# Performance work log

Hardware: AMD Instinct MI355X
Metric: run time of the kernel (lower is better)

The kernel has to match this reference:

```python
import jax, jax.numpy as jnp
import numpy as np

N_NODES = 50000
N_EDGES = 500000
IN_DIM = 64
OUT_DIM = 64
NUM_RELS = 16


def setup_inputs() -> dict:
    key = jax.random.key(0)
    ks = jax.random.split(key, 8)
    h = jax.random.normal(ks[0], (N_NODES, IN_DIM), dtype=jnp.float32)
    he = jax.random.normal(ks[1], (N_EDGES, IN_DIM), dtype=jnp.float32)
    src = jax.random.randint(ks[2], (N_EDGES,), 0, N_NODES)
    dst = jax.random.randint(ks[3], (N_EDGES,), 0, N_NODES)
    rel = jax.random.randint(ks[4], (N_EDGES,), 0, NUM_RELS)
    # xavier-ish scales
    W_shared = jax.random.normal(ks[5], (OUT_DIM, IN_DIM), dtype=jnp.float32) * (2.0 / (IN_DIM + OUT_DIM)) ** 0.5
    W_attn = jax.random.normal(ks[6], (1, 3 * OUT_DIM), dtype=jnp.float32) * (2.0 / (3 * OUT_DIM + 1)) ** 0.5
    W_rel = jax.random.normal(ks[7], (NUM_RELS, IN_DIM, OUT_DIM), dtype=jnp.float32) * (2.0 / (IN_DIM + OUT_DIM)) ** 0.5
    return {"h": h, "he": he, "src": src, "dst": dst, "rel": rel,
            "W_shared": W_shared, "W_attn": W_attn, "W_rel": W_rel}


def reference(h, he, src, dst, rel, W_shared, W_attn, W_rel):
    # --- edge attention: a = attn_fc([z_src, z_edge, z_dst]) (raw linear score, no softmax in original) ---
    Z = h @ W_shared.T                      # [N, out] project all nodes once
    ze = he @ W_shared.T                    # [E, out]
    # split attn weight to avoid materializing [E, 3*out] concat
    Wa_s, Wa_e, Wa_d = jnp.split(W_attn, 3, axis=1)   # each [1, out]
    a = Z[src] @ Wa_s.T + ze @ Wa_e.T + Z[dst] @ Wa_d.T   # [E, 1]
    # --- message: msg = (h_src @ W_rel[rel]) * a ---
    # compute per-(node, relation) transform once [N, R, out], then gather per edge
    H_all = jnp.einsum('ni,rio->nro', h, W_rel)          # [N, R, out]
    msg = H_all[src, rel] * a                             # [E, out]
    # --- scatter-sum aggregation into destination nodes ---
    out = jax.ops.segment_sum(msg, dst, num_segments=N_NODES)  # [N, out]
    # apply_func: activation (relu), no bias
    return jax.nn.relu(out)
```

## Files before the change

### kernel.cpp

```cpp
#include <hip/hip_runtime.h>
#include <math.h>

#define N_NODES 50000
#define N_EDGES 500000
#define DIM 64
#define NUM_RELS 16
#define GPB 160


__global__ void k1_node(const float* __restrict__ h,
                        const float* __restrict__ W_shared,
                        const float* __restrict__ W_attn,
                        float* __restrict__ sn, float* __restrict__ dn,
                        float4* __restrict__ out4,
                        int* __restrict__ counts, int* __restrict__ cursor) {
    __shared__ float sus[64], sud[64];
    int t = threadIdx.x;
    if (t < 64) {
        float us = 0.f, ud = 0.f;
        for (int o = 0; o < 64; ++o) {
            float w = W_shared[o * 64 + t];
            us = fmaf(w, W_attn[o],       us);
            ud = fmaf(w, W_attn[128 + o], ud);
        }
        sus[t] = us; sud[t] = ud;
    }
    if (t >= 64 && t < 80)  counts[t - 64] = 0;
    if (t >= 80 && t < 96)  cursor[t - 80] = 0;
    __syncthreads();

    int n = blockIdx.x * blockDim.x + t;
    if (n >= N_NODES) return;
    const float* hp = h + (size_t)n * DIM;
    float s = 0.f, d = 0.f;
#pragma unroll
    for (int i = 0; i < 64; i += 4) {
        float4 v = *(const float4*)(hp + i);
        s = fmaf(v.x, sus[i], s);     s = fmaf(v.y, sus[i + 1], s);
        s = fmaf(v.z, sus[i + 2], s); s = fmaf(v.w, sus[i + 3], s);
        d = fmaf(v.x, sud[i], d);     d = fmaf(v.y, sud[i + 1], d);
        d = fmaf(v.z, sud[i + 2], d); d = fmaf(v.w, sud[i + 3], d);
    }
    sn[n] = s; dn[n] = d;
    float4 z = make_float4(0.f, 0.f, 0.f, 0.f);
#pragma unroll
    for (int i = 0; i < 16; ++i) out4[(size_t)n * 16 + i] = z;
}

__global__ void k2_ae(const float4* __restrict__ he4,
                      const int* __restrict__ src, const int* __restrict__ dst,
                      const int* __restrict__ rel,
                      const float* __restrict__ W_shared,
                      const float* __restrict__ W_attn,
                      const float* __restrict__ sn, const float* __restrict__ dn,
                      float* __restrict__ ae, int* __restrict__ counts) {
    __shared__ float sve[64];
    __shared__ int hist[NUM_RELS];
    int t = threadIdx.x;
    if (t < NUM_RELS) hist[t] = 0;
    if (t < 64) {
        float ve = 0.f;
        for (int o = 0; o < 64; ++o)
            ve = fmaf(W_shared[o * 64 + t], W_attn[64 + o], ve);
        sve[t] = ve;
    }
    __syncthreads();

    const int lane = t & 63;
    const int sub  = lane & 3;
    const int eo   = lane >> 2;
    const int gw   = blockIdx.x * 4 + (t >> 6);
    const int nw   = gridDim.x * 4;

    float4 u0 = *(const float4*)(sve + sub * 16 + 0);
    float4 u1 = *(const float4*)(sve + sub * 16 + 4);
    float4 u2 = *(const float4*)(sve + sub * 16 + 8);
    float4 u3 = *(const float4*)(sve + sub * 16 + 12);

    for (int base = gw * 16; base < N_EDGES; base += nw * 16) {
        int e = base + eo;
        float p = 0.f;
        if (e < N_EDGES) {
            const float4* row = he4 + (size_t)e * 16 + sub * 4;
            float4 a = row[0], b = row[1], c = row[2], d = row[3];
            p = a.x*u0.x + a.y*u0.y + a.z*u0.z + a.w*u0.w
              + b.x*u1.x + b.y*u1.y + b.z*u1.z + b.w*u1.w
              + c.x*u2.x + c.y*u2.y + c.z*u2.z + c.w*u2.w
              + d.x*u3.x + d.y*u3.y + d.z*u3.z + d.w*u3.w;
        }
        p += __shfl_xor(p, 1, 64);
        p += __shfl_xor(p, 2, 64);
        if (sub == 0 && e < N_EDGES) {
            ae[e] = p + sn[src[e]] + dn[dst[e]];
            atomicAdd(&hist[rel[e]], 1);
        }
    }
    __syncthreads();
    if (t < NUM_RELS && hist[t]) atomicAdd(&counts[t], hist[t]);
}

__global__ void k4_scatter(const int* __restrict__ rel,
                           const int* __restrict__ counts,
                           int* __restrict__ cursor,
                           int* __restrict__ perm) {
    __shared__ int hist[NUM_RELS];
    __shared__ int bbase[NUM_RELS];
    __shared__ int soffs[NUM_RELS];
    int t = threadIdx.x;
    if (t < NUM_RELS) hist[t] = 0;
    if (t == 0) {
        int acc = 0;
        for (int j = 0; j < NUM_RELS; ++j) { soffs[j] = acc; acc += counts[j]; }
    }
    __syncthreads();
    int e = blockIdx.x * 1024 + t;
    int r = 0, lpos = 0;
    bool valid = (e < N_EDGES);
    if (valid) { r = rel[e]; lpos = atomicAdd(&hist[r], 1); }
    __syncthreads();
    if (t < NUM_RELS) bbase[t] = hist[t] ? atomicAdd(&cursor[t], hist[t]) : 0;
    __syncthreads();
    if (valid) perm[soffs[r] + bbase[r] + lpos] = e;
}

__global__ __launch_bounds__(256, 4) void k5_main(
    const float* __restrict__ h,
    const int* __restrict__ src, const int* __restrict__ dst,
    const float* __restrict__ W_rel,
    const float* __restrict__ ae,
    const int* __restrict__ counts, const int* __restrict__ perm,
    float* __restrict__ out)
{
    const int lane = threadIdx.x & 63;
    const int wib  = __builtin_amdgcn_readfirstlane(threadIdx.x >> 6);
    const int r    = blockIdx.x & 15;
    const int g    = blockIdx.x >> 4;
    const int wr   = g * 4 + wib;
    const int WPR  = GPB * 4;

    int begin = 0, cr = 0;
#pragma unroll
    for (int j = 0; j < NUM_RELS; ++j) {
        int c = counts[j];
        if (j < r) begin += c;
        if (j == r) cr = c;
    }
    const int end = begin + cr;

    float w[64];
    const float* wb = W_rel + (size_t)r * (DIM * DIM) + lane;
#pragma unroll
    for (int i = 0; i < 64; ++i) w[i] = wb[i * 64];
#pragma unroll
    for (int i = 0; i < 64; ++i) asm volatile("" : "+v"(w[i]));

    for (int base = begin + wr * 64; base < end; base += WPR * 64) {
        int s_l = 0, d_l = 0; float a_l = 0.f;
        if (base + lane < end) {
            int e_l = perm[base + lane];
            s_l = src[e_l];
            d_l = dst[e_l];
            a_l = ae[e_l];
        }
        const int kmax = min(64, end - base);
        int k = 0;
        for (; k + 2 <= kmax; k += 2) {
            const int si0 = __builtin_amdgcn_readlane(s_l, k);
            const int si1 = __builtin_amdgcn_readlane(s_l, k + 1);
            const int di0 = __builtin_amdgcn_readlane(d_l, k);
            const int di1 = __builtin_amdgcn_readlane(d_l, k + 1);
            const float a0 = __int_as_float(__builtin_amdgcn_readlane(__float_as_int(a_l), k));
            const float a1 = __int_as_float(__builtin_amdgcn_readlane(__float_as_int(a_l), k + 1));
            const float* hp0 = h + (size_t)si0 * DIM;
            const float* hp1 = h + (size_t)si1 * DIM;
            float x0 = 0.f, y0 = 0.f, x1 = 0.f, y1 = 0.f;
#pragma unroll
            for (int i = 0; i < 64; i += 2) {
                x0 = fmaf(hp0[i],     w[i],     x0);
                x1 = fmaf(hp1[i],     w[i],     x1);
                y0 = fmaf(hp0[i + 1], w[i + 1], y0);
                y1 = fmaf(hp1[i + 1], w[i + 1], y1);
            }
            unsafeAtomicAdd(out + (size_t)di0 * DIM + lane, a0 * (x0 + y0));
            unsafeAtomicAdd(out + (size_t)di1 * DIM + lane, a1 * (x1 + y1));
        }
        if (k < kmax) {
            const int si = __builtin_amdgcn_readlane(s_l, k);
            const int di = __builtin_amdgcn_readlane(d_l, k);
            const float ak = __int_as_float(__builtin_amdgcn_readlane(__float_as_int(a_l), k));
            const float* hp = h + (size_t)si * DIM;
            float x = 0.f, y = 0.f;
#pragma unroll
            for (int i = 0; i < 64; i += 2) {
                x = fmaf(hp[i],     w[i],     x);
                y = fmaf(hp[i + 1], w[i + 1], y);
            }
            unsafeAtomicAdd(out + (size_t)di * DIM + lane, ak * (x + y));
        }
    }
}

__global__ void k6_relu(float4* __restrict__ out, int n4) {
    int i = blockIdx.x * blockDim.x + threadIdx.x;
    if (i < n4) {
        float4 v = out[i];
        v.x = fmaxf(v.x, 0.f); v.y = fmaxf(v.y, 0.f);
        v.z = fmaxf(v.z, 0.f); v.w = fmaxf(v.w, 0.f);
        out[i] = v;
    }
}

extern "C" void kernel_launch(void* const* d_in, const int* in_sizes, int n_in,
                              void* d_out, int out_size, void* d_ws, size_t ws_size,
                              hipStream_t stream) {
    const float* h        = (const float*)d_in[0];
    const float* he       = (const float*)d_in[1];
    const int*   src      = (const int*)d_in[2];
    const int*   dst      = (const int*)d_in[3];
    const int*   rel      = (const int*)d_in[4];
    const float* W_shared = (const float*)d_in[5];
    const float* W_attn   = (const float*)d_in[6];
    const float* W_rel    = (const float*)d_in[7];
    float*       out      = (float*)d_out;

    int*   counts = (int*)d_ws + 192;
    int*   cursor = (int*)d_ws + 228;
    float* sn     = (float*)d_ws + 256;
    float* dn     = (float*)d_ws + 50256;
    float* ae     = (float*)d_ws + 100256;
    int*   perm   = (int*)d_ws + 600256;

    k1_node<<<(N_NODES + 255) / 256, 256, 0, stream>>>(h, W_shared, W_attn, sn, dn,
                                                       (float4*)out, counts, cursor);
    k2_ae<<<1024, 256, 0, stream>>>((const float4*)he, src, dst, rel, W_shared, W_attn,
                                    sn, dn, ae, counts);
    k4_scatter<<<(N_EDGES + 1023) / 1024, 1024, 0, stream>>>(rel, counts, cursor, perm);
    k5_main<<<NUM_RELS * GPB, 256, 0, stream>>>(h, src, dst, W_rel, ae, counts, perm, out);
    int n4 = out_size / 4;
    k6_relu<<<(n4 + 255) / 256, 256, 0, stream>>>((float4*)out, n4);
}
```

Baseline: 382.7 us.

## Fuse pipeline into one cooperative persistent kernel with packed edge records

Replaces the five separate launches with a single cooperative kernel whose phases are separated by grid-wide syncs, with a multi-launch fallback if the cooperative launch fails. The relation histogram moves into the node phase. The edge-score computation is merged with the counting-sort scatter, and each sorted edge is written as a packed int4 record (src, dst, score) so the main phase needs no indirect perm lookups. The main phase now processes one edge at a time per wave in chunks of 32, reading the record uniformly and prefetching the next one. Fewer launches and less gather traffic are traded for grid-sync overhead, a fixed 1024-block grid that may give lower occupancy, and less per-wave instruction-level parallelism in the main loop.

```diff
diff --git a/kernel.cpp b/kernel.cpp
--- a/kernel.cpp
+++ b/kernel.cpp
@@ -1,21 +1,34 @@
 #include <hip/hip_runtime.h>
+#include <hip/hip_cooperative_groups.h>
 #include <math.h>
+
+namespace cg = cooperative_groups;
 
 #define N_NODES 50000
 #define N_EDGES 500000
 #define DIM 64
 #define NUM_RELS 16
-#define GPB 160
-
-
-__global__ void k1_node(const float* __restrict__ h,
-                        const float* __restrict__ W_shared,
-                        const float* __restrict__ W_attn,
-                        float* __restrict__ sn, float* __restrict__ dn,
-                        float4* __restrict__ out4,
-                        int* __restrict__ counts, int* __restrict__ cursor) {
+#define NBLK 1024
+#define NTHR 256
+
+
+__device__ void phase0(int* counts, int* cursor) {
+    if (blockIdx.x == 0 && threadIdx.x < NUM_RELS) {
+        counts[threadIdx.x] = 0;
+        cursor[threadIdx.x] = 0;
+    }
+}
+
+__device__ void phase1(const float* __restrict__ h,
+                       const float* __restrict__ W_shared,
+                       const float* __restrict__ W_attn,
+                       const int* __restrict__ rel,
+                       float* __restrict__ sn, float* __restrict__ dn,
+                       float4* __restrict__ out4,
+                       int* counts) {
     __shared__ float sus[64], sud[64];
-    int t = threadIdx.x;
+    __shared__ int histp1[NUM_RELS];
+    const int t = threadIdx.x, bid = blockIdx.x;
     if (t < 64) {
         float us = 0.f, ud = 0.f;
         for (int o = 0; o < 64; ++o) {
@@ -25,118 +38,90 @@
         }
         sus[t] = us; sud[t] = ud;
     }
-    if (t >= 64 && t < 80)  counts[t - 64] = 0;
-    if (t >= 80 && t < 96)  cursor[t - 80] = 0;
+    if (t < NUM_RELS) histp1[t] = 0;
     __syncthreads();
 
-    int n = blockIdx.x * blockDim.x + t;
-    if (n >= N_NODES) return;
-    const float* hp = h + (size_t)n * DIM;
-    float s = 0.f, d = 0.f;
-#pragma unroll
-    for (int i = 0; i < 64; i += 4) {
-        float4 v = *(const float4*)(hp + i);
-        s = fmaf(v.x, sus[i], s);     s = fmaf(v.y, sus[i + 1], s);
-        s = fmaf(v.z, sus[i + 2], s); s = fmaf(v.w, sus[i + 3], s);
-        d = fmaf(v.x, sud[i], d);     d = fmaf(v.y, sud[i + 1], d);
-        d = fmaf(v.z, sud[i + 2], d); d = fmaf(v.w, sud[i + 3], d);
-    }
-    sn[n] = s; dn[n] = d;
-    float4 z = make_float4(0.f, 0.f, 0.f, 0.f);
-#pragma unroll
-    for (int i = 0; i < 16; ++i) out4[(size_t)n * 16 + i] = z;
-}
-
-__global__ void k2_ae(const float4* __restrict__ he4,
-                      const int* __restrict__ src, const int* __restrict__ dst,
-                      const int* __restrict__ rel,
-                      const float* __restrict__ W_shared,
-                      const float* __restrict__ W_attn,
-                      const float* __restrict__ sn, const float* __restrict__ dn,
-                      float* __restrict__ ae, int* __restrict__ counts) {
+    for (int n = bid * NTHR + t; n < N_NODES; n += NBLK * NTHR) {
+        const float* hp = h + (size_t)n * DIM;
+        float s = 0.f, d = 0.f;
+#pragma unroll
+        for (int i = 0; i < 64; i += 4) {
+            float4 v = *(const float4*)(hp + i);
+            s = fmaf(v.x, sus[i], s);     s = fmaf(v.y, sus[i + 1], s);
+            s = fmaf(v.z, sus[i + 2], s); s = fmaf(v.w, sus[i + 3], s);
+            d = fmaf(v.x, sud[i], d);     d = fmaf(v.y, sud[i + 1], d);
+            d = fmaf(v.z, sud[i + 2], d); d = fmaf(v.w, sud[i + 3], d);
+        }
+        sn[n] = s; dn[n] = d;
+        float4 z = make_float4(0.f, 0.f, 0.f, 0.f);
+#pragma unroll
+        for (int i = 0; i < 16; ++i) out4[(size_t)n * 16 + i] = z;
+    }
+    for (int e = bid * NTHR + t; e < N_EDGES; e += NBLK * NTHR)
+        atomicAdd(&histp1[rel[e]], 1);
+    __syncthreads();
+    if (t < NUM_RELS && histp1[t]) atomicAdd(&counts[t], histp1[t]);
+}
+
+__device__ void phase2(const float4* __restrict__ he4,
+                       const int* __restrict__ src, const int* __restrict__ dst,
+                       const int* __restrict__ rel,
+                       const float* __restrict__ W_shared,
+                       const float* __restrict__ W_attn,
+                       const float* __restrict__ sn, const float* __restrict__ dn,
+                       const int* counts, int* cursor, int4* __restrict__ rec) {
     __shared__ float sve[64];
-    __shared__ int hist[NUM_RELS];
-    int t = threadIdx.x;
-    if (t < NUM_RELS) hist[t] = 0;
+    __shared__ int hist[NUM_RELS], bbase[NUM_RELS], soffs[NUM_RELS];
+    const int t = threadIdx.x, bid = blockIdx.x;
     if (t < 64) {
         float ve = 0.f;
         for (int o = 0; o < 64; ++o)
             ve = fmaf(W_shared[o * 64 + t], W_attn[64 + o], ve);
         sve[t] = ve;
     }
-    __syncthreads();
-
-    const int lane = t & 63;
-    const int sub  = lane & 3;
-    const int eo   = lane >> 2;
-    const int gw   = blockIdx.x * 4 + (t >> 6);
-    const int nw   = gridDim.x * 4;
-
-    float4 u0 = *(const float4*)(sve + sub * 16 + 0);
-    float4 u1 = *(const float4*)(sve + sub * 16 + 4);
-    float4 u2 = *(const float4*)(sve + sub * 16 + 8);
-    float4 u3 = *(const float4*)(sve + sub * 16 + 12);
-
-    for (int base = gw * 16; base < N_EDGES; base += nw * 16) {
-        int e = base + eo;
-        float p = 0.f;
-        if (e < N_EDGES) {
-            const float4* row = he4 + (size_t)e * 16 + sub * 4;
-            float4 a = row[0], b = row[1], c = row[2], d = row[3];
-            p = a.x*u0.x + a.y*u0.y + a.z*u0.z + a.w*u0.w
-              + b.x*u1.x + b.y*u1.y + b.z*u1.z + b.w*u1.w
-              + c.x*u2.x + c.y*u2.y + c.z*u2.z + c.w*u2.w
-              + d.x*u3.x + d.y*u3.y + d.z*u3.z + d.w*u3.w;
-        }
-        p += __shfl_xor(p, 1, 64);
-        p += __shfl_xor(p, 2, 64);
-        if (sub == 0 && e < N_EDGES) {
-            ae[e] = p + sn[src[e]] + dn[dst[e]];
-            atomicAdd(&hist[rel[e]], 1);
-        }
-    }
-    __syncthreads();
-    if (t < NUM_RELS && hist[t]) atomicAdd(&counts[t], hist[t]);
-}
-
-__global__ void k4_scatter(const int* __restrict__ rel,
-                           const int* __restrict__ counts,
-                           int* __restrict__ cursor,
-                           int* __restrict__ perm) {
-    __shared__ int hist[NUM_RELS];
-    __shared__ int bbase[NUM_RELS];
-    __shared__ int soffs[NUM_RELS];
-    int t = threadIdx.x;
-    if (t < NUM_RELS) hist[t] = 0;
     if (t == 0) {
         int acc = 0;
         for (int j = 0; j < NUM_RELS; ++j) { soffs[j] = acc; acc += counts[j]; }
     }
-    __syncthreads();
-    int e = blockIdx.x * 1024 + t;
-    int r = 0, lpos = 0;
-    bool valid = (e < N_EDGES);
-    if (valid) { r = rel[e]; lpos = atomicAdd(&hist[r], 1); }
-    __syncthreads();
-    if (t < NUM_RELS) bbase[t] = hist[t] ? atomicAdd(&cursor[t], hist[t]) : 0;
-    __syncthreads();
-    if (valid) perm[soffs[r] + bbase[r] + lpos] = e;
-}
-
-__global__ __launch_bounds__(256, 4) void k5_main(
-    const float* __restrict__ h,
-    const int* __restrict__ src, const int* __restrict__ dst,
-    const float* __restrict__ W_rel,
-    const float* __restrict__ ae,
-    const int* __restrict__ counts, const int* __restrict__ perm,
-    float* __restrict__ out)
-{
-    const int lane = threadIdx.x & 63;
-    const int wib  = __builtin_amdgcn_readfirstlane(threadIdx.x >> 6);
-    const int r    = blockIdx.x & 15;
-    const int g    = blockIdx.x >> 4;
+    for (int e0 = bid * NTHR; e0 < N_EDGES; e0 += NBLK * NTHR) {
+        __syncthreads();
+        if (t < NUM_RELS) hist[t] = 0;
+        __syncthreads();
+        int e = e0 + t;
+        bool valid = (e < N_EDGES);
+        int r = 0, lpos = 0, s_ = 0, d_ = 0; float aev = 0.f;
+        if (valid) {
+            s_ = src[e]; d_ = dst[e]; r = rel[e];
+            const float4* hr = he4 + (size_t)e * 16;
+            float acc = 0.f;
+#pragma unroll
+            for (int i = 0; i < 16; ++i) {
+                float4 v = hr[i];
+                float4 u = *(const float4*)(sve + 4 * i);
+                acc += v.x * u.x + v.y * u.y + v.z * u.z + v.w * u.w;
+            }
+            aev = acc + sn[s_] + dn[d_];
+            lpos = atomicAdd(&hist[r], 1);
+        }
+        __syncthreads();
+        if (t < NUM_RELS) bbase[t] = hist[t] ? atomicAdd(&cursor[t], hist[t]) : 0;
+        __syncthreads();
+        if (valid) rec[soffs[r] + bbase[r] + lpos] =
+                       make_int4(s_, d_, __float_as_int(aev), 0);
+    }
+}
+
+__device__ void phase3(const float* __restrict__ h,
+                       const float* __restrict__ W_rel,
+                       const int* counts, const int4* __restrict__ rec,
+                       float* __restrict__ out) {
+    const int t = threadIdx.x, bid = blockIdx.x;
+    const int lane = t & 63;
+    const int wib  = __builtin_amdgcn_readfirstlane(t >> 6);
+    const int r    = bid & 15;
+    const int g    = bid >> 4;
     const int wr   = g * 4 + wib;
-    const int WPR  = GPB * 4;
+    const int WPR  = 256;
 
     int begin = 0, cr = 0;
 #pragma unroll
@@ -145,7 +130,8 @@
         if (j < r) begin += c;
         if (j == r) cr = c;
     }
-    const int end = begin + cr;
+    begin = __builtin_amdgcn_readfirstlane(begin);
+    const int end = __builtin_amdgcn_readfirstlane(begin + cr);
 
     float w[64];
     const float* wb = W_rel + (size_t)r * (DIM * DIM) + lane;
@@ -154,88 +140,111 @@
 #pragma unroll
     for (int i = 0; i < 64; ++i) asm volatile("" : "+v"(w[i]));
 
-    for (int base = begin + wr * 64; base < end; base += WPR * 64) {
-        int s_l = 0, d_l = 0; float a_l = 0.f;
-        if (base + lane < end) {
-            int e_l = perm[base + lane];
-            s_l = src[e_l];
-            d_l = dst[e_l];
-            a_l = ae[e_l];
-        }
-        const int kmax = min(64, end - base);
-        int k = 0;
-        for (; k + 2 <= kmax; k += 2) {
-            const int si0 = __builtin_amdgcn_readlane(s_l, k);
-            const int si1 = __builtin_amdgcn_readlane(s_l, k + 1);
-            const int di0 = __builtin_amdgcn_readlane(d_l, k);
-            const int di1 = __builtin_amdgcn_readlane(d_l, k + 1);
-            const float a0 = __int_as_float(__builtin_amdgcn_readlane(__float_as_int(a_l), k));
-            const float a1 = __int_as_float(__builtin_amdgcn_readlane(__float_as_int(a_l), k + 1));
-            const float* hp0 = h + (size_t)si0 * DIM;
-            const float* hp1 = h + (size_t)si1 * DIM;
-            float x0 = 0.f, y0 = 0.f, x1 = 0.f, y1 = 0.f;
-#pragma unroll
-            for (int i = 0; i < 64; i += 2) {
-                x0 = fmaf(hp0[i],     w[i],     x0);
-                x1 = fmaf(hp1[i],     w[i],     x1);
-                y0 = fmaf(hp0[i + 1], w[i + 1], y0);
-                y1 = fmaf(hp1[i + 1], w[i + 1], y1);
+    const int C = 32;
+    for (int base = begin + wr * C; base < end; base += WPR * C) {
+        const int lim = (base + C < end) ? base + C : end;
+        int4 rv = rec[base];
+        for (int k = base; k < lim; ++k) {
+            const int kn = (k + 1 < lim) ? k + 1 : k;
+            int4 rvn = rec[kn];
+            const int   si = __builtin_amdgcn_readfirstlane(rv.x);
+            const int   di = __builtin_amdgcn_readfirstlane(rv.y);
+            const float ak = __int_as_float(__builtin_amdgcn_readfirstlane(rv.z));
+            const float* hp = h + (size_t)si * DIM;
+            float a0 = 0.f, a1 = 0.f, a2 = 0.f, a3 = 0.f;
+#pragma unroll
+            for (int i = 0; i < 64; i += 4) {
+                a0 = fmaf(hp[i],     w[i],     a0);
+                a1 = fmaf(hp[i + 1], w[i + 1], a1);
+                a2 = fmaf(hp[i + 2], w[i + 2], a2);
+                a3 = fmaf(hp[i + 3], w[i + 3], a3);
             }
-            unsafeAtomicAdd(out + (size_t)di0 * DIM + lane, a0 * (x0 + y0));
-            unsafeAtomicAdd(out + (size_t)di1 * DIM + lane, a1 * (x1 + y1));
-        }
-        if (k < kmax) {
-            const int si = __builtin_amdgcn_readlane(s_l, k);
-            const int di = __builtin_amdgcn_readlane(d_l, k);
-            const float ak = __int_as_float(__builtin_amdgcn_readlane(__float_as_int(a_l), k));
-            const float* hp = h + (size_t)si * DIM;
-            float x = 0.f, y = 0.f;
-#pragma unroll
-            for (int i = 0; i < 64; i += 2) {
-                x = fmaf(hp[i],     w[i],     x);
-                y = fmaf(hp[i + 1], w[i + 1], y);
-            }
-            unsafeAtomicAdd(out + (size_t)di * DIM + lane, ak * (x + y));
-        }
-    }
-}
-
-__global__ void k6_relu(float4* __restrict__ out, int n4) {
-    int i = blockIdx.x * blockDim.x + threadIdx.x;
-    if (i < n4) {
-        float4 v = out[i];
+            unsafeAtomicAdd(out + (size_t)di * DIM + lane,
+                            ak * ((a0 + a1) + (a2 + a3)));
+            rv = rvn;
+        }
+    }
+}
+
+__device__ void phase4(float4* __restrict__ out4) {
+    const int t = threadIdx.x, bid = blockIdx.x;
+    for (int i = bid * NTHR + t; i < N_NODES * 16; i += NBLK * NTHR) {
+        float4 v = out4[i];
         v.x = fmaxf(v.x, 0.f); v.y = fmaxf(v.y, 0.f);
         v.z = fmaxf(v.z, 0.f); v.w = fmaxf(v.w, 0.f);
-        out[i] = v;
-    }
+        out4[i] = v;
+    }
+}
+
+__global__ __launch_bounds__(NTHR, 4) void mega(
+    const float* h, const float4* he4,
+    const int* src, const int* dst, const int* rel,
+    const float* W_shared, const float* W_attn, const float* W_rel,
+    float* out, int* counts, int* cursor,
+    float* sn, float* dn, int4* rec) {
+    cg::grid_group grid = cg::this_grid();
+    phase0(counts, cursor);
+    grid.sync();
+    phase1(h, W_shared, W_attn, rel, sn, dn, (float4*)out, counts);
+    grid.sync();
+    phase2(he4, src, dst, rel, W_shared, W_attn, sn, dn, counts, cursor, rec);
+    grid.sync();
+    phase3(h, W_rel, counts, rec, out);
+    grid.sync();
+    phase4((float4*)out);
+}
+
+__global__ void kz(int* counts, int* cursor) {
+    if (threadIdx.x < NUM_RELS) { counts[threadIdx.x] = 0; cursor[threadIdx.x] = 0; }
+}
+__global__ __launch_bounds__(NTHR, 4) void kp1(const float* h, const float* Ws,
+    const float* Wa, const int* rel, float* sn, float* dn, float* out,
+    int* counts) {
+    phase1(h, Ws, Wa, rel, sn, dn, (float4*)out, counts);
+}
+__global__ __launch_bounds__(NTHR, 4) void kp2(const float4* he4, const int* src,
+    const int* dst, const int* rel, const float* Ws, const float* Wa,
+    const float* sn, const float* dn, const int* counts, int* cursor, int4* rec) {
+    phase2(he4, src, dst, rel, Ws, Wa, sn, dn, counts, cursor, rec);
+}
+__global__ __launch_bounds__(NTHR, 4) void kp3(const float* h, const float* W_rel,
+    const int* counts, const int4* rec, float* out) {
+    phase3(h, W_rel, counts, rec, out);
+}
+__global__ __launch_bounds__(NTHR, 4) void kp4(float* out) {
+    phase4((float4*)out);
 }
 
 extern "C" void kernel_launch(void* const* d_in, const int* in_sizes, int n_in,
                               void* d_out, int out_size, void* d_ws, size_t ws_size,
                               hipStream_t stream) {
-    const float* h        = (const float*)d_in[0];
-    const float* he       = (const float*)d_in[1];
-    const int*   src      = (const int*)d_in[2];
-    const int*   dst      = (const int*)d_in[3];
-    const int*   rel      = (const int*)d_in[4];
-    const float* W_shared = (const float*)d_in[5];
-    const float* W_attn   = (const float*)d_in[6];
-    const float* W_rel    = (const float*)d_in[7];
-    float*       out      = (float*)d_out;
+    const float*  h        = (const float*)d_in[0];
+    const float4* he4      = (const float4*)d_in[1];
+    const int*    src      = (const int*)d_in[2];
+    const int*    dst      = (const int*)d_in[3];
+    const int*    rel      = (const int*)d_in[4];
+    const float*  W_shared = (const float*)d_in[5];
+    const float*  W_attn   = (const float*)d_in[6];
+    const float*  W_rel    = (const float*)d_in[7];
+    float*        out      = (float*)d_out;
 
     int*   counts = (int*)d_ws + 192;
     int*   cursor = (int*)d_ws + 228;
     float* sn     = (float*)d_ws + 256;
     float* dn     = (float*)d_ws + 50256;
-    float* ae     = (float*)d_ws + 100256;
-    int*   perm   = (int*)d_ws + 600256;
-
-    k1_node<<<(N_NODES + 255) / 256, 256, 0, stream>>>(h, W_shared, W_attn, sn, dn,
-                                                       (float4*)out, counts, cursor);
-    k2_ae<<<1024, 256, 0, stream>>>((const float4*)he, src, dst, rel, W_shared, W_attn,
-                                    sn, dn, ae, counts);
-    k4_scatter<<<(N_EDGES + 1023) / 1024, 1024, 0, stream>>>(rel, counts, cursor, perm);
-    k5_main<<<NUM_RELS * GPB, 256, 0, stream>>>(h, src, dst, W_rel, ae, counts, perm, out);
-    int n4 = out_size / 4;
-    k6_relu<<<(n4 + 255) / 256, 256, 0, stream>>>((float4*)out, n4);
-}
+    int4*  rec    = (int4*)((int*)d_ws + 100352);
+
+    void* args[] = { (void*)&h, (void*)&he4, (void*)&src, (void*)&dst, (void*)&rel,
+                     (void*)&W_shared, (void*)&W_attn, (void*)&W_rel, (void*)&out,
+                     (void*)&counts, (void*)&cursor, (void*)&sn, (void*)&dn, (void*)&rec };
+
+    hipError_t err = hipLaunchCooperativeKernel((void*)mega, dim3(NBLK), dim3(NTHR),
+                                                args, 0, stream);
+    if (err != hipSuccess) {
+        kz<<<1, 64, 0, stream>>>(counts, cursor);
+        kp1<<<NBLK, NTHR, 0, stream>>>(h, W_shared, W_attn, rel, sn, dn, out, counts);
+        kp2<<<NBLK, NTHR, 0, stream>>>(he4, src, dst, rel, W_shared, W_attn, sn, dn, counts, cursor, rec);
+        kp3<<<NBLK, NTHR, 0, stream>>>(h, W_rel, counts, rec, out);
+        kp4<<<NBLK, NTHR, 0, stream>>>(out);
+    }
+}
```

Measured after the change: 1.010 ms. 164% more time.
